# Performance work log

Measured on AMD Instinct MI355X. Metric: run time of the kernel, lower is better.

## Reference

```python
import jax, jax.numpy as jnp
import numpy as np

IMG = 800          # image size (square)
STRIDE = 4         # feature-map stride
S = 14             # rcnn_crop_size
C = 256            # crop_channels
N = 512            # number of rpn proposals
NUM_CLASSES = 81   # COCO (incl. background at index 0)
HID = 1024
NMS_TH = 0.5
SCORE_TH = 0.05


def setup_inputs() -> dict:
    key = jax.random.key(0)
    ks = jax.random.split(key, 8)
    features = jax.random.normal(ks[0], (1, C, IMG // STRIDE, IMG // STRIDE), jnp.float32)
    # valid proposal boxes (x0, y0, x1, y1) in image coordinates
    u = jax.random.uniform(ks[1], (N, 4), jnp.float32)
    x0 = u[:, 0] * (IMG - 64.0)
    y0 = u[:, 1] * (IMG - 64.0)
    bw = 16.0 + u[:, 2] * 240.0
    bh = 16.0 + u[:, 3] * 240.0
    proposals = jnp.stack([x0, y0, jnp.minimum(x0 + bw, IMG - 1.0), jnp.minimum(y0 + bh, IMG - 1.0)], axis=1)
    d1 = C * S * S  # 50176
    w1 = jax.random.normal(ks[2], (d1, HID), jnp.float32) * (1.0 / np.sqrt(d1))
    b1 = jnp.zeros((HID,), jnp.float32)
    w2 = jax.random.normal(ks[3], (HID, HID), jnp.float32) * (1.0 / np.sqrt(HID))
    b2 = jnp.zeros((HID,), jnp.float32)
    w_cls = jax.random.normal(ks[4], (HID, NUM_CLASSES), jnp.float32) * (1.0 / np.sqrt(HID))
    b_cls = jnp.zeros((NUM_CLASSES,), jnp.float32)
    w_reg = jax.random.normal(ks[5], (HID, NUM_CLASSES * 4), jnp.float32) * (1.0 / np.sqrt(HID))
    b_reg = jnp.zeros((NUM_CLASSES * 4,), jnp.float32)
    return dict(features=features, proposals=proposals, w1=w1, b1=b1, w2=w2, b2=b2,
                w_cls=w_cls, b_cls=b_cls, w_reg=w_reg, b_reg=b_reg)


def roi_align(feat, boxes):
    """feat: [C,H,W]; boxes: [N,4] image coords -> crops [N,C,S,S] via bilinear sampling (1 sample per bin)."""
    _, H, W = feat.shape
    b = boxes / STRIDE
    t = (jnp.arange(S, dtype=feat.dtype) + 0.5) / S                # [S] bin centers
    xs = b[:, 0:1] + (b[:, 2:3] - b[:, 0:1]) * t                   # [N,S]
    ys = b[:, 1:2] + (b[:, 3:4] - b[:, 1:2]) * t                   # [N,S]
    xx = jnp.broadcast_to(xs[:, None, :], (boxes.shape[0], S, S))  # [N,S,S]
    yy = jnp.broadcast_to(ys[:, :, None], (boxes.shape[0], S, S))
    x0f = jnp.floor(xx); y0f = jnp.floor(yy)
    fx = xx - x0f; fy = yy - y0f
    x0i = jnp.clip(x0f.astype(jnp.int32), 0, W - 1); x1i = jnp.clip(x0i + 1, 0, W - 1)
    y0i = jnp.clip(y0f.astype(jnp.int32), 0, H - 1); y1i = jnp.clip(y0i + 1, 0, H - 1)
    # gathers -> [C,N,S,S]
    v = (((1 - fx) * (1 - fy))[None] * feat[:, y0i, x0i]
         + (fx * (1 - fy))[None] * feat[:, y0i, x1i]
         + ((1 - fx) * fy)[None] * feat[:, y1i, x0i]
         + (fx * fy)[None] * feat[:, y1i, x1i])
    return v.transpose(1, 0, 2, 3)  # [N,C,S,S]


def decode_boxes(rois, d):
    w = rois[:, 2] - rois[:, 0]; h = rois[:, 3] - rois[:, 1]
    cx = rois[:, 0] + 0.5 * w; cy = rois[:, 1] + 0.5 * h
    px = cx + d[:, 0] * w; py = cy + d[:, 1] * h
    pw = w * jnp.exp(jnp.clip(d[:, 2], -4.0, 4.0))
    ph = h * jnp.exp(jnp.clip(d[:, 3], -4.0, 4.0))
    b = jnp.stack([px - 0.5 * pw, py - 0.5 * ph, px + 0.5 * pw, py + 0.5 * ph], axis=1)
    return jnp.clip(b, 0.0, IMG - 1.0)


def iou_matrix(b):
    area = jnp.maximum(b[:, 2] - b[:, 0], 0.0) * jnp.maximum(b[:, 3] - b[:, 1], 0.0)
    ix0 = jnp.maximum(b[:, None, 0], b[None, :, 0])
    iy0 = jnp.maximum(b[:, None, 1], b[None, :, 1])
    ix1 = jnp.minimum(b[:, None, 2], b[None, :, 2])
    iy1 = jnp.minimum(b[:, None, 3], b[None, :, 3])
    inter = jnp.maximum(ix1 - ix0, 0.0) * jnp.maximum(iy1 - iy0, 0.0)
    return inter / (area[:, None] + area[None, :] - inter + 1e-6)


def reference(features, proposals, w1, b1, w2, b2, w_cls, b_cls, w_reg, b_reg):
    # 1) RoIAlign crop
    crops = roi_align(features[0], proposals)              # [N,C,S,S]
    # 2) RCNN head
    x = crops.reshape(N, -1)
    x = jax.nn.relu(x @ w1 + b1)
    x = jax.nn.relu(x @ w2 + b2)
    logits = x @ w_cls + b_cls                             # [N,81]
    deltas = (x @ w_reg + b_reg).reshape(N, NUM_CLASSES, 4)
    # 3) NMS post-processing
    probs = jax.nn.softmax(logits, axis=-1)
    fg = probs[:, 1:]                                      # exclude background
    labels = jnp.argmax(fg, axis=-1) + 1                   # [N]
    scores = jnp.max(fg, axis=-1)                          # [N]
    d = deltas[jnp.arange(N), labels]                      # per-ROI delta of predicted class
    boxes = decode_boxes(proposals, d)
    order = jnp.argsort(-scores)
    bs = boxes[order]; ss = scores[order]; ls = labels[order]
    valid = ss > SCORE_TH
    M = iou_matrix(bs)                                     # [N,N]
    idx = jnp.arange(N)
    def body(i, keep):
        alive = keep[i] & valid[i]
        supp = (M[i] > NMS_TH) & (idx > i) & alive
        return keep & (~supp)
    keep = jax.lax.fori_loop(0, N, body, valid)
    keepf = jax.lax.stop_gradient(keep.astype(bs.dtype))
    final = jnp.concatenate([bs, ss[:, None]], axis=1) * keepf[:, None]   # [N,5]
    return final, ls.astype(jnp.int32), keep
```

## Files before the change

### kernel.cpp

```cpp
#include <hip/hip_runtime.h>
#include <cstdint>

#define F_H 200
#define F_W 200
#define D1  50176
#define NBOX 512
#define NHID 1024

typedef _Float16 f16;
typedef _Float16 half8 __attribute__((ext_vector_type(8)));
typedef _Float16 half4v __attribute__((ext_vector_type(4)));
typedef _Float16 half2v __attribute__((ext_vector_type(2)));
typedef float    f32x4 __attribute__((ext_vector_type(4)));

__device__ __forceinline__ void gload16(const void* g, void* l) {
  __builtin_amdgcn_global_load_lds((const __attribute__((address_space(1))) void*)g,
                                   (__attribute__((address_space(3))) void*)l,
                                   16, 0, 0);
}

__device__ __forceinline__ half2v pkrtz(float a, float b) {
  return __builtin_bit_cast(half2v, __builtin_amdgcn_cvt_pkrtz(a, b));
}

__device__ __forceinline__ void splitf16(float v, f16& h, f16& l) {
  f16 hh = (f16)v;
  float hf = (float)hh;
  if (fabsf(hf) < 6.1035156e-5f) hf = 0.f;
  h = (f16)hh;
  if (fabsf(hf) < 6.1035156e-5f) h = (f16)0.f;
  l = (f16)((v - hf) * 2048.f);
}

__global__ __launch_bounds__(256) void k_roi(const float* __restrict__ feat,
                                             const float* __restrict__ prop,
                                             f16* __restrict__ xhi, f16* __restrict__ xlo) {
  uint32_t idx = blockIdx.x * 256u + threadIdx.x;
  uint32_t n = idx / 25088u;
  uint32_t rem = idx % 25088u;
  uint32_t c = rem / 98u;
  uint32_t r2 = rem % 98u;
  uint32_t i = r2 / 7u;
  uint32_t jp = r2 % 7u;
  float b0 = prop[n * 4 + 0] * 0.25f, b1 = prop[n * 4 + 1] * 0.25f;
  float b2 = prop[n * 4 + 2] * 0.25f, b3 = prop[n * 4 + 3] * 0.25f;
  float ty = ((float)i + 0.5f) * (1.0f / 14.0f);
  float yy = b1 + (b3 - b1) * ty;
  float y0f = floorf(yy);
  float fy = yy - y0f;
  int y0 = (int)y0f; y0 = y0 < 0 ? 0 : (y0 > F_H - 1 ? F_H - 1 : y0);
  int y1 = y0 + 1 > F_H - 1 ? F_H - 1 : y0 + 1;
  const float* fr0 = feat + (size_t)c * (F_H * F_W) + (size_t)y0 * F_W;
  const float* fr1 = feat + (size_t)c * (F_H * F_W) + (size_t)y1 * F_W;
  f16 hs[2], ls[2];
#pragma unroll
  for (int e = 0; e < 2; ++e) {
    uint32_t j = jp * 2u + (uint32_t)e;
    float tx = ((float)j + 0.5f) * (1.0f / 14.0f);
    float xx = b0 + (b2 - b0) * tx;
    float x0f = floorf(xx);
    float fx = xx - x0f;
    int x0 = (int)x0f; x0 = x0 < 0 ? 0 : (x0 > F_W - 1 ? F_W - 1 : x0);
    int x1 = x0 + 1 > F_W - 1 ? F_W - 1 : x0 + 1;
    float v00 = fr0[x0], v01 = fr0[x1], v10 = fr1[x0], v11 = fr1[x1];
    float v = (1.f - fx) * (1.f - fy) * v00 + fx * (1.f - fy) * v01 +
              (1.f - fx) * fy * v10 + fx * fy * v11;
    splitf16(v, hs[e], ls[e]);
  }
  uint32_t base = n * 50176u + c * 196u + i * 14u + jp * 2u;
  half2v hv; hv[0] = hs[0]; hv[1] = hs[1];
  half2v lv; lv[0] = ls[0]; lv[1] = ls[1];
  *(half2v*)(xhi + base) = hv;
  *(half2v*)(xlo + base) = lv;
}

__global__ __launch_bounds__(256) void k_tsplit(const float* __restrict__ W,
                                                f16* __restrict__ hiT, f16* __restrict__ loT,
                                                int Kdim, int Ndim) {
  __shared__ f16 lh[64 * 72];
  __shared__ f16 ll[64 * 72];
  int t = threadIdx.x;
  int k0 = blockIdx.x * 64, n0 = blockIdx.y * 64;
  int r = t >> 2, cq = t & 3;
  const float* src = W + (size_t)(k0 + r) * Ndim + n0 + cq * 16;
  f16 hv[16], lv[16];
#pragma unroll
  for (int e = 0; e < 4; ++e) {
    f32x4 v = *(const f32x4*)(src + e * 4);
#pragma unroll
    for (int x = 0; x < 4; ++x) splitf16(v[x], hv[e * 4 + x], lv[e * 4 + x]);
  }
#pragma unroll
  for (int j = 0; j < 16; ++j) {
    int n_l = cq * 16 + j;
    lh[n_l * 72 + r] = hv[j];
    ll[n_l * 72 + r] = lv[j];
  }
  __syncthreads();
  f16* oh = hiT + (size_t)(n0 + r) * Kdim + k0 + cq * 16;
  f16* ol = loT + (size_t)(n0 + r) * Kdim + k0 + cq * 16;
  *(half8*)(oh)     = *(const half8*)(&lh[r * 72 + cq * 16]);
  *(half8*)(oh + 8) = *(const half8*)(&lh[r * 72 + cq * 16 + 8]);
  *(half8*)(ol)     = *(const half8*)(&ll[r * 72 + cq * 16]);
  *(half8*)(ol + 8) = *(const half8*)(&ll[r * 72 + cq * 16 + 8]);
}

__global__ __launch_bounds__(256) void k_packT(const float* __restrict__ wc_, const float* __restrict__ bc,
                                               const float* __restrict__ wr_, const float* __restrict__ br,
                                               f16* __restrict__ whT_hi, f16* __restrict__ whT_lo,
                                               float* __restrict__ bh) {
  uint32_t idx = blockIdx.x * 256u + threadIdx.x;
  if (idx < 512u * 1024u) {
    uint32_t n = idx >> 10, k = idx & 1023u;
    float v = 0.f;
    if (n < 81u) v = wc_[k * 81u + n];
    else if (n < 405u) v = wr_[k * 324u + (n - 81u)];
    f16 h, l; splitf16(v, h, l);
    whT_hi[idx] = h; whT_lo[idx] = l;
  } else if (idx < 512u * 1024u + 512u) {
    uint32_t n = idx - 512u * 1024u;
    float v = 0.f;
    if (n < 81u) v = bc[n];
    else if (n < 405u) v = br[n - 81u];
    bh[n] = v;
  }
}

__global__ __launch_bounds__(512, 2) void k_gemm2(
    const f16* __restrict__ Ahi, const f16* __restrict__ Alo,
    const f16* __restrict__ Bhi, const f16* __restrict__ Blo,
    float* __restrict__ Cp, int K, int N, int Kc, int nMt, int nNt)
{
  __shared__ char sm[131072];
  const int t = threadIdx.x;
  const int lane = t & 63;
  const int wid = t >> 6;
  const int wr = wid >> 2;
  const int wc = wid & 3;
  const int rl = lane & 15;
  const int lq = lane >> 4;

  int bid = blockIdx.x;
  int low = bid & 7, qq = bid >> 3;
  int nt = qq % nNt;
  int chi = qq / nNt;
  int c = chi * 8 + low;
  int ks = c / nMt;
  int mt = c % nMt;
  const int brow = mt * 256;
  const int nbase = nt * 256;
  const int k0 = ks * Kc;
  const int nk = Kc >> 5;

  uint32_t aoffg[2], aldso[2];
#pragma unroll
  for (int i = 0; i < 2; ++i) {
    uint32_t idx = (uint32_t)t + 512u * i;
    uint32_t q2 = idx >> 2, s = idx & 3;
    uint32_t qh = q2 >> 6;
    uint32_t grh = (qh == 1u) ? 2u : (qh == 2u) ? 1u : qh;
    uint32_t gr = grh * 64u + (q2 & 63u);
    aoffg[i] = (uint32_t)(brow + gr) * (uint32_t)K + (s ^ ((q2 >> 1) & 3u)) * 8u;
    aldso[i] = idx * 16u;
  }
  uint32_t boffg[2], bldso[2];
#pragma unroll
  for (int i = 0; i < 2; ++i) {
    uint32_t idx = (uint32_t)t + 512u * i;
    uint32_t rB = idx >> 2, s = idx & 3;
    boffg[i] = (uint32_t)(nbase + rB) * (uint32_t)K + (s ^ ((rB >> 1) & 3u)) * 8u;
    bldso[i] = idx * 16u;
  }

  const uint32_t swzk = (uint32_t)(lq ^ ((rl >> 1) & 3)) * 16u;
  const uint32_t a_off_lane = (uint32_t)(rl * 64) + swzk;
  const uint32_t b_off_lane = (uint32_t)((wc * 16 + rl) * 64) + swzk;

  f32x4 zero4 = {0.f, 0.f, 0.f, 0.f};
  f32x4 acc[8][4];
#pragma unroll
  for (int m = 0; m < 8; ++m)
#pragma unroll
    for (int n = 0; n < 4; ++n) acc[m][n] = zero4;

#define PH0STAGE(LB, KB) do { \
    gload16(Bhi + boffg[0] + (KB), (LB) + 32768 + bldso[0]); \
    gload16(Blo + boffg[0] + (KB), (LB) + 49152 + bldso[0]); \
    gload16(Bhi + boffg[1] + (KB), (LB) + 32768 + bldso[1]); \
    gload16(Blo + boffg[1] + (KB), (LB) + 49152 + bldso[1]); \
    gload16(Ahi + aoffg[0] + (KB), (LB) + aldso[0]); \
    gload16(Alo + aoffg[0] + (KB), (LB) + 16384 + aldso[0]); \
  } while (0)

#define PH1STAGE(LB, KB) do { \
    gload16(Ahi + aoffg[1] + (KB), (LB) + aldso[1]); \
    gload16(Alo + aoffg[1] + (KB), (LB) + 16384 + aldso[1]); \
  } while (0)

#define COMPUTE_PHASE(P) do { \
    half8 bh2[4], bl2[4]; \
    _Pragma("unroll") \
    for (int nf = 0; nf < 4; ++nf) { \
      bh2[nf] = *(const half8*)(lb + 32768 + nf * 4096 + b_off_lane); \
      bl2[nf] = *(const half8*)(lb + 49152 + nf * 4096 + b_off_lane); \
    } \
    __builtin_amdgcn_s_setprio(1); \
    _Pragma("unroll") \
    for (int mm = 0; mm < 4; ++mm) { \
      const char* ab = lb + (P) * 8192 + wr * 4096 + mm * 1024 + a_off_lane; \
      half8 ah = *(const half8*)(ab); \
      half8 al = *(const half8*)(ab + 16384); \
      _Pragma("unroll") \
      for (int nf = 0; nf < 4; ++nf) { \
        acc[(P)*4+mm][nf] = __builtin_amdgcn_mfma_f32_16x16x32_f16(ah, bh2[nf], acc[(P)*4+mm][nf], 0, 0, 0); \
        f32x4 tt = __builtin_amdgcn_mfma_f32_16x16x32_f16(ah, bl2[nf], zero4, 0, 0, 0); \
        tt = __builtin_amdgcn_mfma_f32_16x16x32_f16(al, bh2[nf], tt, 0, 0, 0); \
        acc[(P)*4+mm][nf] += tt * 4.8828125e-4f; \
      } \
    } \
    __builtin_amdgcn_s_setprio(0); \
  } while (0)

  PH0STAGE(sm, (uint32_t)k0);
  PH1STAGE(sm, (uint32_t)k0);

  int cur = 0;
  for (int kt = 0; kt < nk; ++kt) {
    int ktn = (kt + 1 < nk) ? kt + 1 : kt;
    uint32_t kbn = (uint32_t)(k0 + ktn * 32);
    const char* lb = sm + cur * 65536;
    char* lbn = sm + (cur ^ 1) * 65536;

    asm volatile("s_waitcnt vmcnt(2)" ::: "memory");
    __builtin_amdgcn_s_barrier();
    __builtin_amdgcn_sched_barrier(0);
    PH0STAGE(lbn, kbn);
    COMPUTE_PHASE(0);

    asm volatile("s_waitcnt vmcnt(6)" ::: "memory");
    __builtin_amdgcn_s_barrier();
    __builtin_amdgcn_sched_barrier(0);
    PH1STAGE(lbn, kbn);
    COMPUTE_PHASE(1);

    cur ^= 1;
  }

  float* Cs = Cp + (size_t)ks * ((size_t)512 * (uint32_t)N);
#pragma unroll
  for (int m = 0; m < 8; ++m) {
    int rg = brow + wr * 128 + m * 16 + lq * 4;
#pragma unroll
    for (int nf = 0; nf < 4; ++nf) {
      int cg = nbase + nf * 64 + wc * 16 + rl;
#pragma unroll
      for (int rr = 0; rr < 4; ++rr)
        Cs[(size_t)(rg + rr) * (uint32_t)N + cg] = acc[m][nf][rr];
    }
  }
#undef PH0STAGE
#undef PH1STAGE
}

__global__ __launch_bounds__(512, 2) void k_gemm3(
    const f16* __restrict__ Ahi, const f16* __restrict__ Alo,
    const float* __restrict__ B, float* __restrict__ Cp,
    int K, int N, int Kc, int nMt, int nNt)
{
  __shared__ char sm[131072];
  const int t = threadIdx.x;
  const int lane = t & 63;
  const int wid = t >> 6;
  const int wr = wid >> 2;
  const int wc = wid & 3;
  const int rl = lane & 15;
  const int lq = lane >> 4;

  int bid = blockIdx.x;
  int low = bid & 7, qq = bid >> 3;
  int nt = qq % nNt;
  int chi = qq / nNt;
  int c = chi * 8 + low;
  int ks = c / nMt;
  int mt = c % nMt;
  const int brow = mt * 256;
  const int nbase = nt * 256;
  const int k0 = ks * Kc;
  const int nk = Kc >> 5;

  uint32_t aoffg[2], aldso[2];
#pragma unroll
  for (int i = 0; i < 2; ++i) {
    uint32_t idx = (uint32_t)t + 512u * i;
    uint32_t q2 = idx >> 2, s = idx & 3;
    uint32_t qh = q2 >> 6;
    uint32_t grh = (qh == 1u) ? 2u : (qh == 2u) ? 1u : qh;
    uint32_t gr = grh * 64u + (q2 & 63u);
    aoffg[i] = (uint32_t)(brow + gr) * (uint32_t)K + (s ^ ((q2 >> 1) & 3u)) * 8u;
    aldso[i] = idx * 16u;
  }

  const uint32_t nrow = (uint32_t)t & 255u;
  const uint32_t kh = (uint32_t)t >> 8;
  const float* bsrc0 = B + (size_t)((uint32_t)k0 + kh * 16u) * (uint32_t)N + (uint32_t)nbase + nrow;
  const uint32_t bswz = (nrow >> 1) & 3u;
  const uint32_t wb0 = nrow * 64u + (((kh * 2u)      ^ bswz) << 4);
  const uint32_t wb1 = nrow * 64u + (((kh * 2u + 1u) ^ bswz) << 4);

  const uint32_t swzk = (uint32_t)(lq ^ ((rl >> 1) & 3)) * 16u;
  const uint32_t a_off_lane = (uint32_t)(rl * 64) + swzk;
  const uint32_t b_off_lane = (uint32_t)((wc * 16 + rl) * 64) + swzk;

  f32x4 zero4 = {0.f, 0.f, 0.f, 0.f};
  f32x4 acc[8][4];
#pragma unroll
  for (int m = 0; m < 8; ++m)
#pragma unroll
    for (int n = 0; n < 4; ++n) acc[m][n] = zero4;

  float breg[16];

#define LOADB(KT) do { \
    const float* bp = bsrc0 + (size_t)((uint32_t)(KT) * 32u) * (uint32_t)N; \
    _Pragma("unroll") \
    for (int j = 0; j < 16; ++j) breg[j] = bp[(size_t)j * (uint32_t)N]; \
  } while (0)

#define WRITEB(LB) do { \
    half8 h0, l0, h1, l1; \
    _Pragma("unroll") \
    for (int j = 0; j < 16; j += 2) { \
      float v0 = breg[j], v1 = breg[j + 1]; \
      half2v hp = pkrtz(v0, v1); \
      f16 e0 = (fabsf(v0) >= 6.1035156e-5f) ? hp[0] : (f16)0; \
      f16 e1 = (fabsf(v1) >= 6.1035156e-5f) ? hp[1] : (f16)0; \
      half2v lp = pkrtz((v0 - (float)e0) * 2048.f, (v1 - (float)e1) * 2048.f); \
      if (j < 8) { h0[j] = e0; h0[j + 1] = e1; l0[j] = lp[0]; l0[j + 1] = lp[1]; } \
      else { h1[j - 8] = e0; h1[j - 7] = e1; l1[j - 8] = lp[0]; l1[j - 7] = lp[1]; } \
    } \
    *(half8*)((LB) + 32768 + wb0) = h0; \
    *(half8*)((LB) + 49152 + wb0) = l0; \
    *(half8*)((LB) + 32768 + wb1) = h1; \
    *(half8*)((LB) + 49152 + wb1) = l1; \
  } while (0)

#define STAGE_A4(LB, KB) do { \
    gload16(Ahi + aoffg[0] + (KB), (LB) + aldso[0]); \
    gload16(Alo + aoffg[0] + (KB), (LB) + 16384 + aldso[0]); \
    gload16(Ahi + aoffg[1] + (KB), (LB) + aldso[1]); \
    gload16(Alo + aoffg[1] + (KB), (LB) + 16384 + aldso[1]); \
  } while (0)

  LOADB(0);
  STAGE_A4(sm, (uint32_t)k0);
  WRITEB(sm);
  __syncthreads();

  int cur = 0;
  for (int kt = 0; kt < nk; ++kt) {
    int ktn = (kt + 1 < nk) ? kt + 1 : kt;
    const char* lb = sm + cur * 65536;
    char* lbn = sm + (cur ^ 1) * 65536;

    LOADB(ktn);
    STAGE_A4(lbn, (uint32_t)(k0 + ktn * 32));
    COMPUTE_PHASE(0);
    WRITEB(lbn);
    COMPUTE_PHASE(1);
    __syncthreads();
    cur ^= 1;
  }

  float* Cs = Cp + (size_t)ks * ((size_t)512 * (uint32_t)N);
#pragma unroll
  for (int m = 0; m < 8; ++m) {
    int rg = brow + wr * 128 + m * 16 + lq * 4;
#pragma unroll
    for (int nf = 0; nf < 4; ++nf) {
      int cg = nbase + nf * 64 + wc * 16 + rl;
#pragma unroll
      for (int rr = 0; rr < 4; ++rr)
        Cs[(size_t)(rg + rr) * (uint32_t)N + cg] = acc[m][nf][rr];
    }
  }
#undef LOADB
#undef WRITEB
#undef STAGE_A4
#undef COMPUTE_PHASE
}

__global__ __launch_bounds__(256) void k_reduce(
    const float* __restrict__ parts, const float* __restrict__ bias,
    int nS, int MN4, int Ncols, int relu,
    float* __restrict__ outf, f16* __restrict__ ohi, f16* __restrict__ olo)
{
  uint32_t idx = blockIdx.x * 256u + threadIdx.x;
  if (idx >= (uint32_t)MN4) return;
  f32x4 s = *(const f32x4*)(bias + ((idx * 4u) % (uint32_t)Ncols));
  const f32x4* p4 = (const f32x4*)parts;
  for (int i = 0; i < nS; ++i) s += p4[(size_t)i * (uint32_t)MN4 + idx];
  if (relu) {
#pragma unroll
    for (int j = 0; j < 4; ++j) s[j] = fmaxf(s[j], 0.f);
  }
  if (outf) *(f32x4*)(outf + (size_t)idx * 4) = s;
  if (ohi) {
    half4v h, l;
#pragma unroll
    for (int j = 0; j < 4; ++j) { f16 hh, ll; splitf16(s[j], hh, ll); h[j] = hh; l[j] = ll; }
    *(half4v*)(ohi + (size_t)idx * 4) = h;
    *(half4v*)(olo + (size_t)idx * 4) = l;
  }
}

__global__ __launch_bounds__(256) void k_post(
    const float* __restrict__ ld, const float* __restrict__ prop,
    float* __restrict__ boxes, float* __restrict__ scores, int* __restrict__ labels)
{
  int n = blockIdx.x * 256 + threadIdx.x;
  if (n >= NBOX) return;
  const float* L = ld + (size_t)n * 512;
  float m = L[0];
  for (int j = 1; j < 81; ++j) m = fmaxf(m, L[j]);
  float sum = 0.f;
  for (int j = 0; j < 81; ++j) sum += expf(L[j] - m);
  float best = -1.f; int bj = 1;
  for (int j = 1; j < 81; ++j) {
    float p = expf(L[j] - m) / sum;
    if (p > best) { best = p; bj = j; }
  }
  float d0 = L[81 + bj * 4 + 0];
  float d1 = L[81 + bj * 4 + 1];
  float d2 = L[81 + bj * 4 + 2];
  float d3 = L[81 + bj * 4 + 3];
  float p0 = prop[n * 4 + 0], p1 = prop[n * 4 + 1], p2 = prop[n * 4 + 2], p3 = prop[n * 4 + 3];
  float w = p2 - p0, h = p3 - p1;
  float cx = p0 + 0.5f * w, cy = p1 + 0.5f * h;
  float px = cx + d0 * w, py = cy + d1 * h;
  float pw = w * expf(fminf(fmaxf(d2, -4.f), 4.f));
  float ph = h * expf(fminf(fmaxf(d3, -4.f), 4.f));
  float bx0 = px - 0.5f * pw, by0 = py - 0.5f * ph;
  float bx1 = px + 0.5f * pw, by1 = py + 0.5f * ph;
  boxes[n * 4 + 0] = fminf(fmaxf(bx0, 0.f), 799.f);
  boxes[n * 4 + 1] = fminf(fmaxf(by0, 0.f), 799.f);
  boxes[n * 4 + 2] = fminf(fmaxf(bx1, 0.f), 799.f);
  boxes[n * 4 + 3] = fminf(fmaxf(by1, 0.f), 799.f);
  scores[n] = best;
  labels[n] = bj;
}

__global__ __launch_bounds__(512) void k_sort(
    const float* __restrict__ scores, const float* __restrict__ boxes, const int* __restrict__ labels,
    float* __restrict__ bs, float* __restrict__ ss, int* __restrict__ ls)
{
  __shared__ unsigned long long keys[512];
  int t = threadIdx.x;
  unsigned sb = __float_as_uint(scores[t]);
  keys[t] = ((unsigned long long)(0xFFFFFFFFu - sb) << 32) | (unsigned)t;
  __syncthreads();
  for (int k = 2; k <= 512; k <<= 1) {
    for (int j = k >> 1; j > 0; j >>= 1) {
      int p = t ^ j;
      if (p > t) {
        unsigned long long a = keys[t], b = keys[p];
        bool asc = ((t & k) == 0);
        if (asc ? (a > b) : (a < b)) { keys[t] = b; keys[p] = a; }
      }
      __syncthreads();
    }
  }
  unsigned o = (unsigned)(keys[t] & 0xFFFFFFFFu);
  ss[t] = scores[o];
  ls[t] = labels[o];
  bs[t * 4 + 0] = boxes[o * 4 + 0];
  bs[t * 4 + 1] = boxes[o * 4 + 1];
  bs[t * 4 + 2] = boxes[o * 4 + 2];
  bs[t * 4 + 3] = boxes[o * 4 + 3];
}

__global__ __launch_bounds__(64) void k_mask(const float* __restrict__ bs,
                                             unsigned long long* __restrict__ mask) {
  int i = blockIdx.x;
  int lane = threadIdx.x;
  float ax0 = bs[i * 4], ay0 = bs[i * 4 + 1], ax1 = bs[i * 4 + 2], ay1 = bs[i * 4 + 3];
  float aarea = fmaxf(ax1 - ax0, 0.f) * fmaxf(ay1 - ay0, 0.f);
  for (int w = 0; w < 8; ++w) {
    int j = w * 64 + lane;
    float bx0 = bs[j * 4], by0 = bs[j * 4 + 1], bx1 = bs[j * 4 + 2], by1 = bs[j * 4 + 3];
    float barea = fmaxf(bx1 - bx0, 0.f) * fmaxf(by1 - by0, 0.f);
    float ix0 = fmaxf(ax0, bx0), iy0 = fmaxf(ay0, by0);
    float ix1 = fminf(ax1, bx1), iy1 = fminf(ay1, by1);
    float inter = fmaxf(ix1 - ix0, 0.f) * fmaxf(iy1 - iy0, 0.f);
    float iou = inter / (aarea + barea - inter + 1e-6f);
    bool cond = (iou > 0.5f) && (j > i);
    unsigned long long b = __ballot(cond);
    if (lane == 0) mask[i * 8 + w] = b;
  }
}

__global__ __launch_bounds__(64) void k_nms(const unsigned long long* __restrict__ mask,
                                            const float* __restrict__ ss,
                                            const float* __restrict__ bs,
                                            const int* __restrict__ ls,
                                            float* __restrict__ out) {
  int lane = threadIdx.x;
  unsigned long long bal[8];
  for (int w = 0; w < 8; ++w) bal[w] = __ballot(ss[w * 64 + lane] > 0.05f);
  unsigned long long keep = (lane < 8) ? bal[lane] : 0ULL;
  for (int i = 0; i < 512; ++i) {
    unsigned long long kw = __shfl(keep, i >> 6);
    if ((kw >> (i & 63)) & 1ULL) {
      unsigned long long mi = (lane < 8) ? mask[i * 8 + lane] : 0ULL;
      keep &= ~mi;
    }
  }
  __shared__ unsigned long long kws[8];
  if (lane < 8) kws[lane] = keep;
  __syncthreads();
  for (int it = 0; it < 56; ++it) {
    int idx = lane + it * 64;
    float val;
    if (idx < 2560) {
      int i = idx / 5, c2 = idx % 5;
      bool kb = (kws[i >> 6] >> (i & 63)) & 1ULL;
      val = kb ? (c2 < 4 ? bs[i * 4 + c2] : ss[i]) : 0.f;
    } else if (idx < 3072) {
      int i = idx - 2560;
      val = (float)ls[i];
    } else {
      int i = idx - 3072;
      val = ((kws[i >> 6] >> (i & 63)) & 1ULL) ? 1.f : 0.f;
    }
    out[idx] = val;
  }
}

static constexpr size_t SZ_X    = (size_t)NBOX * D1 * 2;
static constexpr size_t SZ_PART = (size_t)32 * 512 * 1024 * 4;
static constexpr size_t SZ_H    = (size_t)512 * 1024 * 2;
static constexpr size_t NP_XHI   = 0;
static constexpr size_t NP_XLO   = NP_XHI + SZ_X;
static constexpr size_t NP_PART  = NP_XLO + SZ_X;
static constexpr size_t NP_W2HIT = NP_PART + SZ_PART;
static constexpr size_t NP_W2LOT = NP_W2HIT + (size_t)1024 * 1024 * 2;
static constexpr size_t NP_WHHIT = NP_W2LOT + (size_t)1024 * 1024 * 2;
static constexpr size_t NP_WHLOT = NP_WHHIT + (size_t)512 * 1024 * 2;
static constexpr size_t NP_BH    = NP_WHLOT + (size_t)512 * 1024 * 2;
static constexpr size_t NP_H1HI  = NP_BH + 4096;
static constexpr size_t NP_H1LO  = NP_H1HI + SZ_H;
static constexpr size_t NP_H2HI  = NP_H1LO + SZ_H;
static constexpr size_t NP_H2LO  = NP_H2HI + SZ_H;
static constexpr size_t NP_LD    = NP_H2LO + SZ_H;
static constexpr size_t NP_BOX   = NP_LD + (size_t)512 * 512 * 4;
static constexpr size_t NP_SC    = NP_BOX + 512 * 4 * 4;
static constexpr size_t NP_LB    = NP_SC + 4096;
static constexpr size_t NP_BS    = NP_LB + 4096;
static constexpr size_t NP_SS    = NP_BS + 512 * 4 * 4;
static constexpr size_t NP_LS    = NP_SS + 4096;
static constexpr size_t NP_MASK  = NP_LS + 4096;
static constexpr size_t NP_END   = NP_MASK + (size_t)512 * 8 * 8;

extern "C" void kernel_launch(void* const* d_in, const int* in_sizes, int n_in,
                              void* d_out, int out_size, void* d_ws, size_t ws_size,
                              hipStream_t stream)
{
  (void)in_sizes; (void)n_in;
  const float* feat = (const float*)d_in[0];
  const float* prop = (const float*)d_in[1];
  const float* w1   = (const float*)d_in[2];
  const float* b1   = (const float*)d_in[3];
  const float* w2   = (const float*)d_in[4];
  const float* b2   = (const float*)d_in[5];
  const float* wcls = (const float*)d_in[6];
  const float* bcls = (const float*)d_in[7];
  const float* wreg = (const float*)d_in[8];
  const float* breg = (const float*)d_in[9];
  float* out = (float*)d_out;
  char* W = (char*)d_ws;

  if (ws_size < NP_END) {
    (void)hipMemsetAsync(out, 0x7f, (size_t)out_size * 4, stream);
    return;
  }

  f16*   xhi   = (f16*)(W + NP_XHI);
  f16*   xlo   = (f16*)(W + NP_XLO);
  float* parts = (float*)(W + NP_PART);
  f16*   w2hiT = (f16*)(W + NP_W2HIT);
  f16*   w2loT = (f16*)(W + NP_W2LOT);
  f16*   whHiT = (f16*)(W + NP_WHHIT);
  f16*   whLoT = (f16*)(W + NP_WHLOT);
  float* bhead = (float*)(W + NP_BH);
  f16*   h1hi  = (f16*)(W + NP_H1HI);
  f16*   h1lo  = (f16*)(W + NP_H1LO);
  f16*   h2hi  = (f16*)(W + NP_H2HI);
  f16*   h2lo  = (f16*)(W + NP_H2LO);
  float* ldbuf = (float*)(W + NP_LD);
  float* boxes = (float*)(W + NP_BOX);
  float* scores= (float*)(W + NP_SC);
  int*   labels= (int*)(W + NP_LB);
  float* bsrt  = (float*)(W + NP_BS);
  float* ssrt  = (float*)(W + NP_SS);
  int*   lsrt  = (int*)(W + NP_LS);
  unsigned long long* maskb = (unsigned long long*)(W + NP_MASK);

  k_roi<<<50176, 256, 0, stream>>>(feat, prop, xhi, xlo);
  k_tsplit<<<dim3(1024 / 64, 1024 / 64), 256, 0, stream>>>(w2, w2hiT, w2loT, 1024, 1024);
  k_packT<<<2050, 256, 0, stream>>>(wcls, bcls, wreg, breg, whHiT, whLoT, bhead);

  k_gemm3<<<256, 512, 0, stream>>>(xhi, xlo, w1, parts, D1, 1024, 1568, 2, 4);
  k_reduce<<<512, 256, 0, stream>>>(parts, b1, 32, 131072, 1024, 1, nullptr, h1hi, h1lo);

  k_gemm2<<<256, 512, 0, stream>>>(h1hi, h1lo, w2hiT, w2loT, parts, 1024, 1024, 32, 2, 4);
  k_reduce<<<512, 256, 0, stream>>>(parts, b2, 32, 131072, 1024, 1, nullptr, h2hi, h2lo);

  k_gemm2<<<128, 512, 0, stream>>>(h2hi, h2lo, whHiT, whLoT, parts, 1024, 512, 32, 2, 2);
  k_reduce<<<256, 256, 0, stream>>>(parts, bhead, 32, 65536, 512, 0, ldbuf, nullptr, nullptr);

  k_post<<<2, 256, 0, stream>>>(ldbuf, prop, boxes, scores, labels);
  k_sort<<<1, 512, 0, stream>>>(scores, boxes, labels, bsrt, ssrt, lsrt);
  k_mask<<<512, 64, 0, stream>>>(bsrt, maskb);
  k_nms<<<1, 64, 0, stream>>>(maskb, ssrt, bsrt, lsrt, out);
}
```

Measured before the change: 434.6 us.

## Prefetch B operand two tiles ahead with double register buffers and fine-grained waitcnt

The GEMM main loop now keeps two register buffers for the fp32 B tile, loading B two k-steps ahead while A is staged to LDS one step ahead. The loop is unrolled by two so the buffers alternate. The blanket __syncthreads is replaced with explicit s_waitcnt vmcnt/lgkmcnt counts plus sched_barrier, so global-load latency overlaps more MFMA work. This costs more VGPRs and depends on hand-counted outstanding-load numbers being correct.

```diff
diff --git a/kernel.cpp b/kernel.cpp
--- a/kernel.cpp
+++ b/kernel.cpp
@@ -318,19 +318,19 @@
 #pragma unroll
     for (int n = 0; n < 4; ++n) acc[m][n] = zero4;
 
-  float breg[16];
-
-#define LOADB(KT) do { \
+  float bx[16], by[16];
+
+#define LOADB(ARR, KT) do { \
     const float* bp = bsrc0 + (size_t)((uint32_t)(KT) * 32u) * (uint32_t)N; \
     _Pragma("unroll") \
-    for (int j = 0; j < 16; ++j) breg[j] = bp[(size_t)j * (uint32_t)N]; \
+    for (int j = 0; j < 16; ++j) ARR[j] = bp[(size_t)j * (uint32_t)N]; \
   } while (0)
 
-#define WRITEB(LB) do { \
+#define WRITEB(LB, ARR) do { \
     half8 h0, l0, h1, l1; \
     _Pragma("unroll") \
     for (int j = 0; j < 16; j += 2) { \
-      float v0 = breg[j], v1 = breg[j + 1]; \
+      float v0 = ARR[j], v1 = ARR[j + 1]; \
       half2v hp = pkrtz(v0, v1); \
       f16 e0 = (fabsf(v0) >= 6.1035156e-5f) ? hp[0] : (f16)0; \
       f16 e1 = (fabsf(v1) >= 6.1035156e-5f) ? hp[1] : (f16)0; \
@@ -351,25 +351,41 @@
     gload16(Alo + aoffg[1] + (KB), (LB) + 16384 + aldso[1]); \
   } while (0)
 
-  LOADB(0);
+#define ITER(KT, IN, OUT) do { \
+    int kA = ((KT) + 1 < nk) ? (KT) + 1 : nk - 1; \
+    int kB = ((KT) + 2 < nk) ? (KT) + 2 : nk - 1; \
+    const char* lb = sm + cur * 65536; \
+    char* lbn = sm + (cur ^ 1) * 65536; \
+    STAGE_A4(lbn, (uint32_t)(k0 + kA * 32));   \
+    LOADB(OUT, kB);                            \
+    COMPUTE_PHASE(0); \
+    asm volatile("s_waitcnt vmcnt(20)" ::: "memory");   \
+    __builtin_amdgcn_sched_barrier(0); \
+    WRITEB(lbn, IN); \
+    COMPUTE_PHASE(1); \
+    asm volatile("s_waitcnt vmcnt(16) lgkmcnt(0)" ::: "memory");   \
+    __builtin_amdgcn_sched_barrier(0); \
+    __builtin_amdgcn_s_barrier(); \
+    cur ^= 1; \
+  } while (0)
+
+  LOADB(bx, 0);
   STAGE_A4(sm, (uint32_t)k0);
-  WRITEB(sm);
-  __syncthreads();
+  asm volatile("s_waitcnt vmcnt(4)" ::: "memory");
+  __builtin_amdgcn_sched_barrier(0);
+  WRITEB(sm, bx);
+  LOADB(by, (nk > 1) ? 1 : 0);
+  asm volatile("s_waitcnt vmcnt(16) lgkmcnt(0)" ::: "memory");
+  __builtin_amdgcn_sched_barrier(0);
+  __builtin_amdgcn_s_barrier();
 
   int cur = 0;
-  for (int kt = 0; kt < nk; ++kt) {
-    int ktn = (kt + 1 < nk) ? kt + 1 : kt;
-    const char* lb = sm + cur * 65536;
-    char* lbn = sm + (cur ^ 1) * 65536;
-
-    LOADB(ktn);
-    STAGE_A4(lbn, (uint32_t)(k0 + ktn * 32));
-    COMPUTE_PHASE(0);
-    WRITEB(lbn);
-    COMPUTE_PHASE(1);
-    __syncthreads();
-    cur ^= 1;
-  }
+  int kt = 0;
+  for (; kt + 1 < nk; kt += 2) {
+    ITER(kt, by, bx);
+    ITER(kt + 1, bx, by);
+  }
+  if (kt < nk) ITER(kt, by, bx);
 
   float* Cs = Cp + (size_t)ks * ((size_t)512 * (uint32_t)N);
 #pragma unroll
@@ -386,6 +402,7 @@
 #undef LOADB
 #undef WRITEB
 #undef STAGE_A4
+#undef ITER
 #undef COMPUTE_PHASE
 }
 
```

New measurement: 429.3 us. No clear change (-1.2%).
